# Kernel optimization log

Measured on AMD Instinct MI355X. Metric: run time of the kernel, lower is better.

The kernel has to match this reference:

```python
import jax, jax.numpy as jnp
import numpy as np

B, N, FEAT, HID, HEADS = 16, 1024, 512, 1024, 2

def setup_inputs() -> dict:
    key = jax.random.key(0)
    ks = jax.random.split(key, 20)
    s = 0.03
    d = {
        'Fs':  jax.random.normal(ks[0], (B, N, FEAT), jnp.float32),
        'Fq':  jax.random.normal(ks[1], (B, N, FEAT), jnp.float32),
        'Fms': jax.random.normal(ks[2], (B, N, FEAT), jnp.float32),
        'out_dim': N,
        'W1': jax.random.normal(ks[3], (FEAT, FEAT), jnp.float32) * s,
        'W2': jax.random.normal(ks[4], (FEAT, FEAT), jnp.float32) * s,
        'W3': jax.random.normal(ks[5], (FEAT, FEAT), jnp.float32) * s,
        'W4': jax.random.normal(ks[6], (FEAT, FEAT), jnp.float32) * s,
        'W5': jax.random.normal(ks[7], (FEAT, FEAT), jnp.float32) * s,
        'W6': jax.random.normal(ks[8], (FEAT, FEAT), jnp.float32) * s,
        'Wq': jax.random.normal(ks[9], (N, N), jnp.float32) * s,
        'Wk': jax.random.normal(ks[10], (N, N), jnp.float32) * s,
        'Wv': jax.random.normal(ks[11], (N, N), jnp.float32) * s,
        'ln_g': jnp.ones((N,), jnp.float32),
        'ln_b': jnp.zeros((N,), jnp.float32),
        'ffn_w1': jax.random.normal(ks[12], (N, HID), jnp.float32) * s,
        'ffn_w2': jax.random.normal(ks[13], (HID, N), jnp.float32) * s,
        'ffn_ln_g': jnp.ones((N,), jnp.float32),
        'ffn_ln_b': jnp.zeros((N,), jnp.float32),
    }
    return d

def _layernorm(x, g, b, eps):
    mu = x.mean(-1, keepdims=True)
    var = x.var(-1, keepdims=True)
    return (x - mu) * jax.lax.rsqrt(var + eps) * g + b

def _affinity(a, b, Wa, Wb, cl):
    # softmax((a Wa)(b Wb)^T / sqrt(cl)) over last axis
    s = jnp.einsum('bnc,bmc->bnm', a @ Wa, b @ Wb) / jnp.sqrt(jnp.float32(cl))
    return jax.nn.softmax(s, axis=-1)

def reference(Fs, Fq, Fms, out_dim, W1, W2, W3, W4, W5, W6, Wq, Wk, Wv,
              ln_g, ln_b, ffn_w1, ffn_w2, ffn_ln_g, ffn_ln_b):
    ass = _affinity(Fms, Fms, W1, W2, Fms.shape[2])   # [B,N,N]
    asq = _affinity(Fs, Fq, W3, W4, Fs.shape[2])      # [B,N,N]
    aqq = _affinity(Fq, Fq, W5, W6, Fq.shape[2])      # [B,N,N]

    Q, K, V = asq @ Wq, ass @ Wk, asq @ Wv            # [B,N,C], C=N
    Bb, Nn, C = Q.shape
    g = C // HEADS
    def heads(x):
        return x.reshape(Bb, Nn, HEADS, g).transpose(0, 2, 1, 3)  # [B,h,N,g]
    Qs, Ks, Vs = heads(Q), heads(K), heads(V)
    attn = jax.nn.softmax(jnp.einsum('bhqg,bhkg->bhqk', Qs, Ks) / jnp.sqrt(jnp.float32(g)), axis=-1)
    o = jnp.einsum('bhqk,bhkg->bhqg', attn, Vs)
    o = o.transpose(0, 2, 1, 3).reshape(Bb, Nn, C)

    x = _layernorm(o + aqq, ln_g, ln_b, 1e-5)
    y = jnp.maximum(x @ ffn_w1, 0.0) @ ffn_w2 + x     # dropout = identity (eval)
    y = _layernorm(y, ffn_ln_g, ffn_ln_b, 1e-6)
    return y
```

## Files before the change

### kernel.cpp

```cpp
#include <hip/hip_runtime.h>
#include <cstdint>

static constexpr long long Bb = 16, Nn = 1024, FE = 512;
static constexpr long long BN = Bb * Nn;
static constexpr long long E1e = BN * FE;
static constexpr long long E2n = BN * Nn;

static constexpr long long O_WT  = 0;
static constexpr long long SZ_W512 = FE * FE * 2;
static constexpr long long O_WQT = O_WT + 6 * SZ_W512;
static constexpr long long SZ_W1K = Nn * Nn * 2;
static constexpr long long O_WKT = O_WQT + SZ_W1K;
static constexpr long long O_WVT = O_WKT + SZ_W1K;
static constexpr long long O_F1T = O_WVT + SZ_W1K;
static constexpr long long O_F2T = O_F1T + SZ_W1K;
static constexpr long long O_SLOTS = O_F2T + SZ_W1K;
static constexpr long long SLOT = E2n * 2;
static constexpr long long O_S0 = O_SLOTS;
static constexpr long long O_S1 = O_S0 + SLOT;
static constexpr long long O_S2 = O_S1 + SLOT;
static constexpr long long O_E0 = O_S2 + SLOT;
static constexpr long long O_E1 = O_E0 + SLOT;
static constexpr long long O_E2 = O_E1 + SLOT;
static constexpr long long WS_NEED = O_E2 + SLOT;
static constexpr long long O_FMSB = O_E1;
static constexpr long long O_FSB  = O_E1 + E1e * 2;
static constexpr long long O_FQB  = O_E2;
static constexpr long long O_C2   = O_E2 + E1e * 2;

typedef __attribute__((ext_vector_type(8))) short short8;
typedef __attribute__((ext_vector_type(4))) float f32x4;

static __device__ __forceinline__ unsigned short f2bf(float f) {
  union { float f; unsigned u; } x; x.f = f;
  unsigned r = x.u + 0x7FFFu + ((x.u >> 16) & 1u);
  return (unsigned short)(r >> 16);
}
static __device__ __forceinline__ float bf2f(unsigned short h) {
  union { unsigned u; float f; } x; x.u = ((unsigned)h) << 16; return x.f;
}
static __device__ __forceinline__ void gload16(const void* g, void* l) {
  __builtin_amdgcn_global_load_lds(
      (const __attribute__((address_space(1))) unsigned int*)g,
      (__attribute__((address_space(3))) unsigned int*)l, 16, 0, 0);
}

template <int EP>
__global__ __launch_bounds__(256) void gemm_nt(
    const unsigned short* __restrict__ A, long long sA, long long hA, int lda,
    const unsigned short* __restrict__ B, long long sB, long long hB, int ldb,
    void* __restrict__ Cv, long long sC, long long hC, int ldc,
    const void* __restrict__ Rv, long long sR, int K) {
  __shared__ unsigned short lA[128 * 64];
  __shared__ unsigned short lB[64 * 64];
  const int tid = threadIdx.x;
  const int wave = tid >> 6, lane = tid & 63;
  const int wm = wave >> 1, wn = wave & 1;
  const int lrow = lane & 15, quad = lane >> 4;
  const int z = blockIdx.z, z1 = z & 15, z2 = z >> 4;
  const int gy = gridDim.y;
  const int bid = blockIdx.x + gridDim.x * blockIdx.y;
  const int chunk = 8 * gy;
  const int bx = (bid / chunk) * 8 + (bid % 8);
  const int by = (bid % chunk) / 8;
  const long long bm = (long long)bx * 128;
  const long long bn = (long long)by * 64;
  const unsigned short* Ab = A + z1 * sA + z2 * hA + bm * lda;
  const unsigned short* Bbp = B + z1 * sB + z2 * hB + bn * ldb;
  const int srow = lane >> 2;
  const int skol = (lane & 3) * 8;
  const int g0 = wave * 2, g1 = wave * 2 + 1;

  f32x4 acc[4][2];
#pragma unroll
  for (int i = 0; i < 4; ++i)
#pragma unroll
    for (int j = 0; j < 2; ++j) acc[i][j] = (f32x4){0.f, 0.f, 0.f, 0.f};

  for (int k0 = 0; k0 < K; k0 += 64) {
    const unsigned short* Ak = Ab + k0 + skol;
    const unsigned short* Bk = Bbp + k0 + skol;
    gload16(Ak + (long long)(g0 * 16 + srow) * lda,      &lA[g0 * 512 + lane * 8]);
    gload16(Ak + (long long)(g1 * 16 + srow) * lda,      &lA[g1 * 512 + lane * 8]);
    gload16(Ak + (long long)(g0 * 16 + srow) * lda + 32, &lA[4096 + g0 * 512 + lane * 8]);
    gload16(Ak + (long long)(g1 * 16 + srow) * lda + 32, &lA[4096 + g1 * 512 + lane * 8]);
    gload16(Bk + (long long)(wave * 16 + srow) * ldb,      &lB[wave * 512 + lane * 8]);
    gload16(Bk + (long long)(wave * 16 + srow) * ldb + 32, &lB[2048 + wave * 512 + lane * 8]);
    __syncthreads();
#pragma unroll
    for (int p = 0; p < 2; ++p) {
      short8 af[4], bfr[2];
#pragma unroll
      for (int t = 0; t < 4; ++t)
        af[t] = *(const short8*)&lA[p * 4096 + (wm * 64 + t * 16 + lrow) * 32 + quad * 8];
#pragma unroll
      for (int u = 0; u < 2; ++u)
        bfr[u] = *(const short8*)&lB[p * 2048 + (wn * 32 + u * 16 + lrow) * 32 + quad * 8];
#pragma unroll
      for (int mt = 0; mt < 4; ++mt)
#pragma unroll
        for (int nt = 0; nt < 2; ++nt)
          acc[mt][nt] = __builtin_amdgcn_mfma_f32_16x16x32_bf16(af[mt], bfr[nt], acc[mt][nt], 0, 0, 0);
    }
    __syncthreads();
  }
  const long long cm = bm + wm * 64, cn = bn + wn * 32;
  const long long cz = z1 * sC + z2 * hC;
#pragma unroll
  for (int mt = 0; mt < 4; ++mt) {
#pragma unroll
    for (int nt = 0; nt < 2; ++nt) {
      long long col = cn + nt * 16 + lrow;
      long long row0 = cm + mt * 16 + quad * 4;
#pragma unroll
      for (int r = 0; r < 4; ++r) {
        long long row = row0 + r;
        float v = acc[mt][nt][r];
        long long idx = cz + row * ldc + col;
        if (EP == 1) ((unsigned short*)Cv)[idx] = f2bf(v);
        else if (EP == 2) ((unsigned short*)Cv)[idx] = f2bf(v > 0.f ? v : 0.f);
        else {
          float rr = bf2f(((const unsigned short*)Rv)[z1 * sR + row * ldc + col]);
          ((float*)Cv)[idx] = v + rr;
        }
      }
    }
  }
}

__global__ __launch_bounds__(256) void cast3_k(const float* __restrict__ i0,
                                               const float* __restrict__ i1,
                                               const float* __restrict__ i2,
                                               unsigned short* o0, unsigned short* o1,
                                               unsigned short* o2) {
  const float* in = (blockIdx.y == 0) ? i0 : (blockIdx.y == 1) ? i1 : i2;
  unsigned short* out = (blockIdx.y == 0) ? o0 : (blockIdx.y == 1) ? o1 : o2;
  long long i = (long long)blockIdx.x * 256 + threadIdx.x;
  float4 v = ((const float4*)in)[i];
  ushort4 o; o.x = f2bf(v.x); o.y = f2bf(v.y); o.z = f2bf(v.z); o.w = f2bf(v.w);
  ((ushort4*)out)[i] = o;
}

__global__ __launch_bounds__(256) void tcast6_k(const float* p0, const float* p1,
                                                const float* p2, const float* p3,
                                                const float* p4, const float* p5,
                                                unsigned short* outb, int rows, int cols) {
  const float* src[6] = {p0, p1, p2, p3, p4, p5};
  const float* in = src[blockIdx.z];
  unsigned short* out = outb + (long long)blockIdx.z * rows * cols;
  __shared__ float t[32][33];
  const int c0 = blockIdx.x * 32, r0 = blockIdx.y * 32;
  const int tx = threadIdx.x, ty = threadIdx.y;
#pragma unroll
  for (int i = 0; i < 4; ++i) {
    int r = r0 + ty + i * 8;
    t[ty + i * 8][tx] = in[(long long)r * cols + c0 + tx];
  }
  __syncthreads();
#pragma unroll
  for (int i = 0; i < 4; ++i) {
    int c = c0 + ty + i * 8;
    out[(long long)c * rows + r0 + tx] = f2bf(t[tx][ty + i * 8]);
  }
}

__global__ __launch_bounds__(256) void softmax_bf(unsigned short* __restrict__ S, float scale) {
  __shared__ float redA[4], redB[4];
  const long long row = blockIdx.x;
  const int t = threadIdx.x, wave = t >> 6, lane = t & 63;
  ushort4 u = ((ushort4*)(S + row * 1024))[t];
  float v0 = bf2f(u.x) * scale, v1 = bf2f(u.y) * scale, v2 = bf2f(u.z) * scale, v3 = bf2f(u.w) * scale;
  float m = fmaxf(fmaxf(v0, v1), fmaxf(v2, v3));
#pragma unroll
  for (int o = 32; o; o >>= 1) m = fmaxf(m, __shfl_down(m, o));
  if (lane == 0) redA[wave] = m;
  __syncthreads();
  m = fmaxf(fmaxf(redA[0], redA[1]), fmaxf(redA[2], redA[3]));
  float e0 = __expf(v0 - m), e1 = __expf(v1 - m), e2 = __expf(v2 - m), e3 = __expf(v3 - m);
  float s = e0 + e1 + e2 + e3;
#pragma unroll
  for (int o = 32; o; o >>= 1) s += __shfl_down(s, o);
  if (lane == 0) redB[wave] = s;
  __syncthreads();
  s = redB[0] + redB[1] + redB[2] + redB[3];
  float inv = 1.f / s;
  ushort4 ob; ob.x = f2bf(e0 * inv); ob.y = f2bf(e1 * inv); ob.z = f2bf(e2 * inv); ob.w = f2bf(e3 * inv);
  ((ushort4*)(S + row * 1024))[t] = ob;
}

__global__ __launch_bounds__(256) void ln1_k(const unsigned short* __restrict__ O,
                                             const unsigned short* __restrict__ Aq,
                                             const float* __restrict__ g, const float* __restrict__ b,
                                             unsigned short* __restrict__ xb) {
  __shared__ float redA[4], redB[4];
  const long long row = blockIdx.x;
  const int t = threadIdx.x, wave = t >> 6, lane = t & 63;
  ushort4 ou = ((const ushort4*)(O + row * 1024))[t];
  ushort4 au = ((const ushort4*)(Aq + row * 1024))[t];
  float v0 = bf2f(ou.x) + bf2f(au.x), v1 = bf2f(ou.y) + bf2f(au.y);
  float v2 = bf2f(ou.z) + bf2f(au.z), v3 = bf2f(ou.w) + bf2f(au.w);
  float s = v0 + v1 + v2 + v3;
  float q = v0 * v0 + v1 * v1 + v2 * v2 + v3 * v3;
#pragma unroll
  for (int o = 32; o; o >>= 1) { s += __shfl_down(s, o); q += __shfl_down(q, o); }
  if (lane == 0) { redA[wave] = s; redB[wave] = q; }
  __syncthreads();
  float S = redA[0] + redA[1] + redA[2] + redA[3];
  float Q = redB[0] + redB[1] + redB[2] + redB[3];
  float mu = S * (1.f / 1024.f);
  float var = Q * (1.f / 1024.f) - mu * mu;
  float rs = rsqrtf(var + 1e-5f);
  float4 gg = ((const float4*)g)[t], bbv = ((const float4*)b)[t];
  ushort4 ob;
  ob.x = f2bf((v0 - mu) * rs * gg.x + bbv.x);
  ob.y = f2bf((v1 - mu) * rs * gg.y + bbv.y);
  ob.z = f2bf((v2 - mu) * rs * gg.z + bbv.z);
  ob.w = f2bf((v3 - mu) * rs * gg.w + bbv.w);
  ((ushort4*)(xb + row * 1024))[t] = ob;
}

__global__ __launch_bounds__(256) void ln2_k(const float* __restrict__ Y,
                                             const float* __restrict__ g, const float* __restrict__ b,
                                             float* __restrict__ out, float eps) {
  __shared__ float redA[4], redB[4];
  const long long row = blockIdx.x;
  const int t = threadIdx.x, wave = t >> 6, lane = t & 63;
  float4 v = ((const float4*)(Y + row * 1024))[t];
  float s = v.x + v.y + v.z + v.w;
  float q = v.x * v.x + v.y * v.y + v.z * v.z + v.w * v.w;
#pragma unroll
  for (int o = 32; o; o >>= 1) { s += __shfl_down(s, o); q += __shfl_down(q, o); }
  if (lane == 0) { redA[wave] = s; redB[wave] = q; }
  __syncthreads();
  float S = redA[0] + redA[1] + redA[2] + redA[3];
  float Q = redB[0] + redB[1] + redB[2] + redB[3];
  float mu = S * (1.f / 1024.f);
  float var = Q * (1.f / 1024.f) - mu * mu;
  float rs = rsqrtf(var + eps);
  float4 gg = ((const float4*)g)[t], bbv = ((const float4*)b)[t];
  float4 o;
  o.x = (v.x - mu) * rs * gg.x + bbv.x;
  o.y = (v.y - mu) * rs * gg.y + bbv.y;
  o.z = (v.z - mu) * rs * gg.z + bbv.z;
  o.w = (v.w - mu) * rs * gg.w + bbv.w;
  ((float4*)(out + row * 1024))[t] = o;
}

extern "C" void kernel_launch(void* const* d_in, const int* in_sizes, int n_in,
                              void* d_out, int out_size, void* d_ws, size_t ws_size,
                              hipStream_t stream) {
  (void)in_sizes; (void)n_in; (void)out_size;
  if (ws_size < (size_t)WS_NEED) return;

  const float* Fs  = (const float*)d_in[0];
  const float* Fq  = (const float*)d_in[1];
  const float* Fms = (const float*)d_in[2];
  const float* Wm[6] = {(const float*)d_in[4], (const float*)d_in[5], (const float*)d_in[6],
                        (const float*)d_in[7], (const float*)d_in[8], (const float*)d_in[9]};
  const float* Wq = (const float*)d_in[10];
  const float* Wk = (const float*)d_in[11];
  const float* Wv = (const float*)d_in[12];
  const float* ln_g = (const float*)d_in[13];
  const float* ln_b = (const float*)d_in[14];
  const float* fw1 = (const float*)d_in[15];
  const float* fw2 = (const float*)d_in[16];
  const float* fg = (const float*)d_in[17];
  const float* fb = (const float*)d_in[18];
  float* out = (float*)d_out;
  uint8_t* ws = (uint8_t*)d_ws;
  auto U16 = [&](long long off) { return (unsigned short*)(ws + off); };

  const float inv_sqrt512 = 0.04419417382415922f;
  dim3 blk(256);

  auto gemm = [&](int ep, const unsigned short* A, long long sA, long long hA, int lda,
                  const unsigned short* B, long long sB, long long hB, int ldb,
                  void* C, long long sC, long long hC, int ldc, const void* R, long long sR,
                  int M, int N, int K, int batch) {
    dim3 g(M / 128, N / 64, batch);
    switch (ep) {
      case 1: gemm_nt<1><<<g, blk, 0, stream>>>(A, sA, hA, lda, B, sB, hB, ldb, C, sC, hC, ldc, R, sR, K); break;
      case 2: gemm_nt<2><<<g, blk, 0, stream>>>(A, sA, hA, lda, B, sB, hB, ldb, C, sC, hC, ldc, R, sR, K); break;
      default: gemm_nt<3><<<g, blk, 0, stream>>>(A, sA, hA, lda, B, sB, hB, ldb, C, sC, hC, ldc, R, sR, K); break;
    }
  };

  tcast6_k<<<dim3(16, 16, 6), dim3(32, 8), 0, stream>>>(
      Wm[0], Wm[1], Wm[2], Wm[3], Wm[4], Wm[5], U16(O_WT), 512, 512);
  tcast6_k<<<dim3(32, 32, 5), dim3(32, 8), 0, stream>>>(
      Wq, Wk, Wv, fw1, fw2, fw2 , U16(O_WQT), 1024, 1024);
  cast3_k<<<dim3(E1e / 4 / 256, 3), blk, 0, stream>>>(
      Fs, Fq, Fms, U16(O_FSB), U16(O_FQB), U16(O_FMSB));

  gemm(1, U16(O_FMSB), 0, 0, 512, U16(O_WT), 0, 0, 512, U16(O_S0), 0, 0, 1024,
       nullptr, 0, (int)BN, 1024, 512, 1);
  gemm(1, U16(O_S0), Nn * 1024, 0, 1024, U16(O_S0) + 512, Nn * 1024, 0, 1024,
       U16(O_E0), Nn * Nn, 0, 1024, nullptr, 0, 1024, 1024, 512, (int)Bb);
  softmax_bf<<<dim3(BN), blk, 0, stream>>>(U16(O_E0), inv_sqrt512);

  gemm(1, U16(O_FSB), 0, 0, 512, U16(O_WT + 2 * SZ_W512), 0, 0, 512, U16(O_C2), 0, 0, 512,
       nullptr, 0, (int)BN, 512, 512, 1);
  gemm(1, U16(O_FQB), 0, 0, 512, U16(O_WT + 3 * SZ_W512), 0, 0, 512, U16(O_S1), 0, 0, 1024,
       nullptr, 0, (int)BN, 1024, 512, 1);
  gemm(1, U16(O_FQB), 0, 0, 512, U16(O_WT + 5 * SZ_W512), 0, 0, 512, U16(O_S2), 0, 0, 512,
       nullptr, 0, (int)BN, 512, 512, 1);
  gemm(1, U16(O_C2), Nn * 512, 0, 512, U16(O_S1), Nn * 1024, 0, 1024,
       U16(O_E1), Nn * Nn, 0, 1024, nullptr, 0, 1024, 1024, 512, (int)Bb);
  softmax_bf<<<dim3(BN), blk, 0, stream>>>(U16(O_E1), inv_sqrt512);
  gemm(1, U16(O_S1) + 512, Nn * 1024, 0, 1024, U16(O_S2), Nn * 512, 0, 512,
       U16(O_E2), Nn * Nn, 0, 1024, nullptr, 0, 1024, 1024, 512, (int)Bb);
  softmax_bf<<<dim3(BN), blk, 0, stream>>>(U16(O_E2), inv_sqrt512);

  const unsigned short* assB = U16(O_E0);
  const unsigned short* asqB = U16(O_E1);

  gemm(1, assB, Nn * Nn, E2n, 1024,
       U16(O_WKT), 0, -(long long)(SZ_W1K / 2), 1024,
       U16(O_S1), Nn * 1024, -(long long)E2n, 1024,
       nullptr, 0, 1024, 1024, 1024, 32);
  gemm(1, U16(O_WVT), 0, 0, 1024, asqB, Nn * Nn, 0, 1024, U16(O_S2), Nn * Nn, 0, 1024,
       nullptr, 0, 1024, 1024, 1024, (int)Bb);

  gemm(1, U16(O_S0), Nn * 1024, 512, 1024, U16(O_S1), Nn * 1024, 512, 1024,
       U16(O_E0), Nn * Nn, 16 * Nn * Nn, 1024, nullptr, 0, 1024, 1024, 512, 32);
  softmax_bf<<<dim3(2 * BN), blk, 0, stream>>>(U16(O_E0), inv_sqrt512);

  gemm(1, U16(O_E0), Nn * Nn, 16 * Nn * Nn, 1024, U16(O_S2), Nn * Nn, 512 * 1024, 1024,
       U16(O_S0), Nn * 1024, 512, 1024, nullptr, 0, 1024, 512, 1024, 32);

  ln1_k<<<dim3(BN), blk, 0, stream>>>(U16(O_S0), U16(O_E2), ln_g, ln_b, U16(O_S1));

  gemm(2, U16(O_S1), 0, 0, 1024, U16(O_F1T), 0, 0, 1024, U16(O_S2), 0, 0, 1024,
       nullptr, 0, (int)BN, 1024, 1024, 1);

  gemm(3, U16(O_S2), 0, 0, 1024, U16(O_F2T), 0, 0, 1024, out, 0, 0, 1024,
       U16(O_S1), 0, (int)BN, 1024, 1024, 1);

  ln2_k<<<dim3(BN), blk, 0, stream>>>(out, fg, fb, out, 1e-6f);
}
```

Baseline: 848.3 us.

## Enlarge GEMM tile to 128x128 and batch projection/affinity GEMMs via offset tables

Result: no change. 848.4 us (+0.0%).

```diff
diff --git a/kernel.cpp b/kernel.cpp
--- a/kernel.cpp
+++ b/kernel.cpp
@@ -26,10 +26,11 @@
 static constexpr long long O_FMSB = O_E1;
 static constexpr long long O_FSB  = O_E1 + E1e * 2;
 static constexpr long long O_FQB  = O_E2;
-static constexpr long long O_C2   = O_E2 + E1e * 2;
 
 typedef __attribute__((ext_vector_type(8))) short short8;
 typedef __attribute__((ext_vector_type(4))) float f32x4;
+
+struct Offs { long long o[6]; };
 
 static __device__ __forceinline__ unsigned short f2bf(float f) {
   union { float f; unsigned u; } x; x.f = f;
@@ -47,69 +48,70 @@
 
 template <int EP>
 __global__ __launch_bounds__(256) void gemm_nt(
-    const unsigned short* __restrict__ A, long long sA, long long hA, int lda,
-    const unsigned short* __restrict__ B, long long sB, long long hB, int ldb,
-    void* __restrict__ Cv, long long sC, long long hC, int ldc,
-    const void* __restrict__ Rv, long long sR, int K) {
-  __shared__ unsigned short lA[128 * 64];
-  __shared__ unsigned short lB[64 * 64];
+    const unsigned short* __restrict__ A, Offs oA, long long sA, int lda,
+    const unsigned short* __restrict__ B, Offs oB, long long sB, int ldb,
+    void* __restrict__ Cv, Offs oC, long long sC, int ldc,
+    const void* __restrict__ Rv, long long sR, int K, int zmsk, int zsh) {
+  __shared__ unsigned short lA[2 * 4096];
+  __shared__ unsigned short lB[2 * 4096];
   const int tid = threadIdx.x;
   const int wave = tid >> 6, lane = tid & 63;
   const int wm = wave >> 1, wn = wave & 1;
   const int lrow = lane & 15, quad = lane >> 4;
-  const int z = blockIdx.z, z1 = z & 15, z2 = z >> 4;
+  const int z = blockIdx.z, z1 = z & zmsk, z2 = z >> zsh;
   const int gy = gridDim.y;
   const int bid = blockIdx.x + gridDim.x * blockIdx.y;
   const int chunk = 8 * gy;
   const int bx = (bid / chunk) * 8 + (bid % 8);
   const int by = (bid % chunk) / 8;
   const long long bm = (long long)bx * 128;
-  const long long bn = (long long)by * 64;
-  const unsigned short* Ab = A + z1 * sA + z2 * hA + bm * lda;
-  const unsigned short* Bbp = B + z1 * sB + z2 * hB + bn * ldb;
+  const long long bn = (long long)by * 128;
+  const unsigned short* Ab = A + oA.o[z2] + z1 * sA + bm * lda;
+  const unsigned short* Bbp = B + oB.o[z2] + z1 * sB + bn * ldb;
   const int srow = lane >> 2;
   const int skol = (lane & 3) * 8;
-  const int g0 = wave * 2, g1 = wave * 2 + 1;
-
-  f32x4 acc[4][2];
+
+  f32x4 acc[4][4];
 #pragma unroll
   for (int i = 0; i < 4; ++i)
 #pragma unroll
-    for (int j = 0; j < 2; ++j) acc[i][j] = (f32x4){0.f, 0.f, 0.f, 0.f};
+    for (int j = 0; j < 4; ++j) acc[i][j] = (f32x4){0.f, 0.f, 0.f, 0.f};
 
   for (int k0 = 0; k0 < K; k0 += 64) {
-    const unsigned short* Ak = Ab + k0 + skol;
-    const unsigned short* Bk = Bbp + k0 + skol;
-    gload16(Ak + (long long)(g0 * 16 + srow) * lda,      &lA[g0 * 512 + lane * 8]);
-    gload16(Ak + (long long)(g1 * 16 + srow) * lda,      &lA[g1 * 512 + lane * 8]);
-    gload16(Ak + (long long)(g0 * 16 + srow) * lda + 32, &lA[4096 + g0 * 512 + lane * 8]);
-    gload16(Ak + (long long)(g1 * 16 + srow) * lda + 32, &lA[4096 + g1 * 512 + lane * 8]);
-    gload16(Bk + (long long)(wave * 16 + srow) * ldb,      &lB[wave * 512 + lane * 8]);
-    gload16(Bk + (long long)(wave * 16 + srow) * ldb + 32, &lB[2048 + wave * 512 + lane * 8]);
+#pragma unroll
+    for (int p = 0; p < 2; ++p) {
+#pragma unroll
+      for (int j = 0; j < 2; ++j) {
+        const int g = wave * 2 + j;
+        gload16(Ab + (long long)(g * 16 + srow) * lda + k0 + p * 32 + skol,
+                &lA[p * 4096 + g * 512 + lane * 8]);
+        gload16(Bbp + (long long)(g * 16 + srow) * ldb + k0 + p * 32 + skol,
+                &lB[p * 4096 + g * 512 + lane * 8]);
+      }
+    }
     __syncthreads();
 #pragma unroll
     for (int p = 0; p < 2; ++p) {
-      short8 af[4], bfr[2];
-#pragma unroll
-      for (int t = 0; t < 4; ++t)
-        af[t] = *(const short8*)&lA[p * 4096 + (wm * 64 + t * 16 + lrow) * 32 + quad * 8];
-#pragma unroll
-      for (int u = 0; u < 2; ++u)
-        bfr[u] = *(const short8*)&lB[p * 2048 + (wn * 32 + u * 16 + lrow) * 32 + quad * 8];
+      short8 af[4], bfr[4];
+#pragma unroll
+      for (int t = 0; t < 4; ++t) {
+        af[t]  = *(const short8*)&lA[p * 4096 + (wm * 64 + t * 16 + lrow) * 32 + quad * 8];
+        bfr[t] = *(const short8*)&lB[p * 4096 + (wn * 64 + t * 16 + lrow) * 32 + quad * 8];
+      }
 #pragma unroll
       for (int mt = 0; mt < 4; ++mt)
 #pragma unroll
-        for (int nt = 0; nt < 2; ++nt)
+        for (int nt = 0; nt < 4; ++nt)
           acc[mt][nt] = __builtin_amdgcn_mfma_f32_16x16x32_bf16(af[mt], bfr[nt], acc[mt][nt], 0, 0, 0);
     }
     __syncthreads();
   }
-  const long long cm = bm + wm * 64, cn = bn + wn * 32;
-  const long long cz = z1 * sC + z2 * hC;
+  const long long cm = bm + wm * 64, cn = bn + wn * 64;
+  const long long cz = oC.o[z2] + z1 * sC;
 #pragma unroll
   for (int mt = 0; mt < 4; ++mt) {
 #pragma unroll
-    for (int nt = 0; nt < 2; ++nt) {
+    for (int nt = 0; nt < 4; ++nt) {
       long long col = cn + nt * 16 + lrow;
       long long row0 = cm + mt * 16 + quad * 4;
 #pragma unroll
@@ -272,16 +274,17 @@
 
   const float inv_sqrt512 = 0.04419417382415922f;
   dim3 blk(256);
-
-  auto gemm = [&](int ep, const unsigned short* A, long long sA, long long hA, int lda,
-                  const unsigned short* B, long long sB, long long hB, int ldb,
-                  void* C, long long sC, long long hC, int ldc, const void* R, long long sR,
-                  int M, int N, int K, int batch) {
-    dim3 g(M / 128, N / 64, batch);
+  const Offs Z0 = {{0, 0, 0, 0, 0, 0}};
+
+  auto gemm = [&](int ep, const unsigned short* A, Offs oA, long long sA, int lda,
+                  const unsigned short* B, Offs oB, long long sB, int ldb,
+                  void* C, Offs oC, long long sC, int ldc, const void* R, long long sR,
+                  int M, int N, int K, int batch, int zmsk, int zsh) {
+    dim3 g(M / 128, N / 128, batch);
     switch (ep) {
-      case 1: gemm_nt<1><<<g, blk, 0, stream>>>(A, sA, hA, lda, B, sB, hB, ldb, C, sC, hC, ldc, R, sR, K); break;
-      case 2: gemm_nt<2><<<g, blk, 0, stream>>>(A, sA, hA, lda, B, sB, hB, ldb, C, sC, hC, ldc, R, sR, K); break;
-      default: gemm_nt<3><<<g, blk, 0, stream>>>(A, sA, hA, lda, B, sB, hB, ldb, C, sC, hC, ldc, R, sR, K); break;
+      case 1: gemm_nt<1><<<g, blk, 0, stream>>>(A, oA, sA, lda, B, oB, sB, ldb, C, oC, sC, ldc, R, sR, K, zmsk, zsh); break;
+      case 2: gemm_nt<2><<<g, blk, 0, stream>>>(A, oA, sA, lda, B, oB, sB, ldb, C, oC, sC, ldc, R, sR, K, zmsk, zsh); break;
+      default: gemm_nt<3><<<g, blk, 0, stream>>>(A, oA, sA, lda, B, oB, sB, ldb, C, oC, sC, ldc, R, sR, K, zmsk, zsh); break;
     }
   };
 
@@ -292,49 +295,57 @@
   cast3_k<<<dim3(E1e / 4 / 256, 3), blk, 0, stream>>>(
       Fs, Fq, Fms, U16(O_FSB), U16(O_FQB), U16(O_FMSB));
 
-  gemm(1, U16(O_FMSB), 0, 0, 512, U16(O_WT), 0, 0, 512, U16(O_S0), 0, 0, 1024,
-       nullptr, 0, (int)BN, 1024, 512, 1);
-  gemm(1, U16(O_S0), Nn * 1024, 0, 1024, U16(O_S0) + 512, Nn * 1024, 0, 1024,
-       U16(O_E0), Nn * Nn, 0, 1024, nullptr, 0, 1024, 1024, 512, (int)Bb);
-  softmax_bf<<<dim3(BN), blk, 0, stream>>>(U16(O_E0), inv_sqrt512);
-
-  gemm(1, U16(O_FSB), 0, 0, 512, U16(O_WT + 2 * SZ_W512), 0, 0, 512, U16(O_C2), 0, 0, 512,
-       nullptr, 0, (int)BN, 512, 512, 1);
-  gemm(1, U16(O_FQB), 0, 0, 512, U16(O_WT + 3 * SZ_W512), 0, 0, 512, U16(O_S1), 0, 0, 1024,
-       nullptr, 0, (int)BN, 1024, 512, 1);
-  gemm(1, U16(O_FQB), 0, 0, 512, U16(O_WT + 5 * SZ_W512), 0, 0, 512, U16(O_S2), 0, 0, 512,
-       nullptr, 0, (int)BN, 512, 512, 1);
-  gemm(1, U16(O_C2), Nn * 512, 0, 512, U16(O_S1), Nn * 1024, 0, 1024,
-       U16(O_E1), Nn * Nn, 0, 1024, nullptr, 0, 1024, 1024, 512, (int)Bb);
-  softmax_bf<<<dim3(BN), blk, 0, stream>>>(U16(O_E1), inv_sqrt512);
-  gemm(1, U16(O_S1) + 512, Nn * 1024, 0, 1024, U16(O_S2), Nn * 512, 0, 512,
-       U16(O_E2), Nn * Nn, 0, 1024, nullptr, 0, 1024, 1024, 512, (int)Bb);
-  softmax_bf<<<dim3(BN), blk, 0, stream>>>(U16(O_E2), inv_sqrt512);
-
-  const unsigned short* assB = U16(O_E0);
-  const unsigned short* asqB = U16(O_E1);
-
-  gemm(1, assB, Nn * Nn, E2n, 1024,
-       U16(O_WKT), 0, -(long long)(SZ_W1K / 2), 1024,
-       U16(O_S1), Nn * 1024, -(long long)E2n, 1024,
-       nullptr, 0, 1024, 1024, 1024, 32);
-  gemm(1, U16(O_WVT), 0, 0, 1024, asqB, Nn * Nn, 0, 1024, U16(O_S2), Nn * Nn, 0, 1024,
-       nullptr, 0, 1024, 1024, 1024, (int)Bb);
-
-  gemm(1, U16(O_S0), Nn * 1024, 512, 1024, U16(O_S1), Nn * 1024, 512, 1024,
-       U16(O_E0), Nn * Nn, 16 * Nn * Nn, 1024, nullptr, 0, 1024, 1024, 512, 32);
+  {
+    Offs oA = {{0, 0, E2n, E2n, E1e, E2n}};
+    Offs oB = {{0, FE * FE, 3 * FE * FE, 4 * FE * FE, 2 * FE * FE, 5 * FE * FE}};
+    Offs oC = {{0, 512, E2n, E2n + 512, 2 * E2n, 2 * E2n + 512}};
+    gemm(1, U16(O_FMSB), oA, 0, 512, U16(O_WT), oB, 0, 512,
+         U16(O_S0), oC, 0, 1024, nullptr, 0, (int)BN, 512, 512, 6, 0, 0);
+  }
+
+  {
+    Offs oA = {{0, 2 * E2n, E2n + 512, 0, 0, 0}};
+    Offs oB = {{512, E2n, 2 * E2n + 512, 0, 0, 0}};
+    Offs oC = {{0, E2n, 2 * E2n, 0, 0, 0}};
+    gemm(1, U16(O_S0), oA, Nn * 1024, 1024, U16(O_S0), oB, Nn * 1024, 1024,
+         U16(O_E0), oC, Nn * Nn, 1024, nullptr, 0, 1024, 1024, 512, 48, 15, 4);
+  }
+  softmax_bf<<<dim3(3 * BN), blk, 0, stream>>>(U16(O_E0), inv_sqrt512);
+
+  {
+    Offs oA = {{0, E2n, 0, 0, 0, 0}};
+    Offs oB = {{0, -(long long)(Nn * Nn), 0, 0, 0, 0}};
+    Offs oC = {{0, -E2n, 0, 0, 0, 0}};
+    gemm(1, U16(O_E0), oA, Nn * Nn, 1024, U16(O_WKT), oB, 0, 1024,
+         U16(O_S1), oC, Nn * 1024, 1024, nullptr, 0, 1024, 1024, 1024, 32, 15, 4);
+  }
+  gemm(1, U16(O_WVT), Z0, 0, 1024, U16(O_E1), Z0, Nn * Nn, 1024,
+       U16(O_S2), Z0, Nn * Nn, 1024, nullptr, 0, 1024, 1024, 1024, 16, 15, 4);
+
+  {
+    Offs oA = {{0, 512, 0, 0, 0, 0}};
+    Offs oB = {{0, 512, 0, 0, 0, 0}};
+    Offs oC = {{0, 16LL * Nn * Nn, 0, 0, 0, 0}};
+    gemm(1, U16(O_S0), oA, Nn * 1024, 1024, U16(O_S1), oB, Nn * 1024, 1024,
+         U16(O_E0), oC, Nn * Nn, 1024, nullptr, 0, 1024, 1024, 512, 32, 15, 4);
+  }
   softmax_bf<<<dim3(2 * BN), blk, 0, stream>>>(U16(O_E0), inv_sqrt512);
 
-  gemm(1, U16(O_E0), Nn * Nn, 16 * Nn * Nn, 1024, U16(O_S2), Nn * Nn, 512 * 1024, 1024,
-       U16(O_S0), Nn * 1024, 512, 1024, nullptr, 0, 1024, 512, 1024, 32);
+  {
+    Offs oA = {{0, 16LL * Nn * Nn, 0, 0, 0, 0}};
+    Offs oB = {{0, 512 * 1024, 0, 0, 0, 0}};
+    Offs oC = {{0, 512, 0, 0, 0, 0}};
+    gemm(1, U16(O_E0), oA, Nn * Nn, 1024, U16(O_S2), oB, Nn * Nn, 1024,
+         U16(O_S0), oC, Nn * 1024, 1024, nullptr, 0, 1024, 512, 1024, 32, 15, 4);
+  }
 
   ln1_k<<<dim3(BN), blk, 0, stream>>>(U16(O_S0), U16(O_E2), ln_g, ln_b, U16(O_S1));
 
-  gemm(2, U16(O_S1), 0, 0, 1024, U16(O_F1T), 0, 0, 1024, U16(O_S2), 0, 0, 1024,
-       nullptr, 0, (int)BN, 1024, 1024, 1);
-
-  gemm(3, U16(O_S2), 0, 0, 1024, U16(O_F2T), 0, 0, 1024, out, 0, 0, 1024,
-       U16(O_S1), 0, (int)BN, 1024, 1024, 1);
+  gemm(2, U16(O_S1), Z0, 0, 1024, U16(O_F1T), Z0, 0, 1024,
+       U16(O_S2), Z0, 0, 1024, nullptr, 0, (int)BN, 1024, 1024, 1, 0, 0);
+
+  gemm(3, U16(O_S2), Z0, 0, 1024, U16(O_F2T), Z0, 0, 1024,
+       out, Z0, 0, 1024, U16(O_S1), 0, (int)BN, 1024, 1024, 1, 0, 0);
 
   ln2_k<<<dim3(BN), blk, 0, stream>>>(out, fg, fb, out, 1e-6f);
 }
```
